# Kernel optimization log

Hardware: AMD Instinct MI355X
Metric: run time of the kernel (lower is better)

Reference implementation:

```python
import jax, jax.numpy as jnp
import numpy as np

N = 100000        # nodes
E = 1_600_000     # edges (avg degree 16)
F_IN = 128        # in_channels
HID = 64          # hidden_channels (per-head)
H1 = 4            # heads layer 1
G = 128           # number of graphs
NEG_SLOPE = 0.2   # PyG GATConv default leaky_relu slope


def setup_inputs() -> dict:
    key = jax.random.key(0)
    ks = jax.random.split(key, 12)
    x = jax.random.normal(ks[0], (N, F_IN), dtype=jnp.float32)
    edge_index = jax.random.randint(ks[1], (2, E), 0, N, dtype=jnp.int64)
    batch = jnp.sort(jax.random.randint(ks[2], (N,), 0, G, dtype=jnp.int64))
    s1 = 1.0 / np.sqrt(F_IN)
    s2 = 1.0 / np.sqrt(H1 * HID)
    # layer 1: in=F_IN, out=H1*HID (PyG lin has no bias; separate bias after concat)
    w1 = jax.random.normal(ks[3], (H1 * HID, F_IN), dtype=jnp.float32) * s1
    a_src1 = jax.random.normal(ks[4], (H1, HID), dtype=jnp.float32) * s1
    a_dst1 = jax.random.normal(ks[5], (H1, HID), dtype=jnp.float32) * s1
    b1 = jnp.zeros((H1 * HID,), dtype=jnp.float32)
    # layer 2: in=H1*HID, out=HID, heads=1
    w2 = jax.random.normal(ks[6], (1 * HID, H1 * HID), dtype=jnp.float32) * s2
    a_src2 = jax.random.normal(ks[7], (1, HID), dtype=jnp.float32) * s2
    a_dst2 = jax.random.normal(ks[8], (1, HID), dtype=jnp.float32) * s2
    b2 = jnp.zeros((HID,), dtype=jnp.float32)
    return {"x": x, "w1": w1, "a_src1": a_src1, "a_dst1": a_dst1, "b1": b1,
            "w2": w2, "a_src2": a_src2, "a_dst2": a_dst2, "b2": b2,
            "edge_index": edge_index, "batch": batch}


def _segment_softmax(alpha, seg, n):
    # numerically-stable softmax of alpha [E,H] grouped by seg (dst node)
    m = jax.ops.segment_max(alpha, seg, num_segments=n)
    m = jnp.where(jnp.isfinite(m), m, 0.0)  # empty segments -> 0
    a = jnp.exp(alpha - m[seg])
    s = jax.ops.segment_sum(a, seg, num_segments=n)
    return a / (s[seg] + 1e-16)


def _gat_conv(x, w, a_src, a_dst, bias, src, dst, n, heads, ch):
    h = (x @ w.T).reshape(n, heads, ch)          # [N,H,C]
    alpha_src = jnp.sum(h * a_src[None], axis=-1)  # [N,H]
    alpha_dst = jnp.sum(h * a_dst[None], axis=-1)  # [N,H]
    e = jax.nn.leaky_relu(alpha_src[src] + alpha_dst[dst], NEG_SLOPE)  # [E,H]
    att = _segment_softmax(e, dst, n)             # [E,H]
    msg = h[src] * att[:, :, None]                # [E,H,C]
    out = jax.ops.segment_sum(msg, dst, num_segments=n)  # [N,H,C]
    return out.reshape(n, heads * ch) + bias


def reference(x, w1, a_src1, a_dst1, b1, w2, a_src2, a_dst2, b2, edge_index, batch):
    src, dst = edge_index[0], edge_index[1]
    h = jax.nn.relu(_gat_conv(x, w1, a_src1, a_dst1, b1, src, dst, N, H1, HID))
    h = jax.nn.relu(_gat_conv(h, w2, a_src2, a_dst2, b2, src, dst, N, 1, HID))
    # global_mean_pool over graph ids
    sums = jax.ops.segment_sum(h, batch, num_segments=G)            # [G,HID]
    cnt = jax.ops.segment_sum(jnp.ones((N,), h.dtype), batch, num_segments=G)
    return sums / jnp.maximum(cnt, 1.0)[:, None]
```

## Files before the change

### kernel.cpp

```cpp
#include <hip/hip_runtime.h>
#include <math.h>
#include <type_traits>

#define NNODES 100000
#define NEDGES 1600000
#define NGRAPH 128
#define NBKT 391
#define CAP 1536
#define EPB 2048

typedef _Float16 f16x4 __attribute__((ext_vector_type(4)));
typedef _Float16 f16x8 __attribute__((ext_vector_type(8)));
typedef float f32x4 __attribute__((ext_vector_type(4)));

__global__ void convert_w(const float* __restrict__ w1, const float* __restrict__ w2,
                          _Float16* __restrict__ w1h, _Float16* __restrict__ w2h) {
  int i = blockIdx.x * 256 + threadIdx.x;
  if (i < 256 * 128) w1h[i] = (_Float16)w1[i];
  int j = i - 256 * 128;
  if (j >= 0 && j < 64 * 256) w2h[j] = (_Float16)w2[j];
}

template <int K, int N, int BN, typename AT>
__global__ __launch_bounds__(256) void gemm_mfma(const AT* __restrict__ A,
    const _Float16* __restrict__ Bh, _Float16* __restrict__ C, int M,
    const float* __restrict__ a_src, const float* __restrict__ a_dst,
    float* __restrict__ asrc, float* __restrict__ adst) {
  constexpr int H = N / 64;
  constexpr int HB = BN / 64;
  constexpr int KS = K / 32, NT = BN / 16;
  const int lane = threadIdx.x & 63, wid = threadIdx.x >> 6;
  const int lr = lane & 15;
  const int lk = (lane >> 4) * 8;
  const int row = blockIdx.x * 64 + wid * 16 + lr;
  const int bn0 = blockIdx.y * BN;
  const int hoff = blockIdx.y * HB;

  f16x8 a[KS];
  if (row < M) {
    const AT* arow = A + (size_t)row * K;
#pragma unroll
    for (int ks = 0; ks < KS; ++ks) {
      if constexpr (std::is_same<AT, float>::value) {
        float4 v0 = *(const float4*)&arow[ks * 32 + lk];
        float4 v1 = *(const float4*)&arow[ks * 32 + lk + 4];
        f16x8 t;
        t[0] = (_Float16)v0.x; t[1] = (_Float16)v0.y; t[2] = (_Float16)v0.z; t[3] = (_Float16)v0.w;
        t[4] = (_Float16)v1.x; t[5] = (_Float16)v1.y; t[6] = (_Float16)v1.z; t[7] = (_Float16)v1.w;
        a[ks] = t;
      } else {
        a[ks] = *(const f16x8*)&arow[ks * 32 + lk];
      }
    }
  } else {
#pragma unroll
    for (int ks = 0; ks < KS; ++ks) a[ks] = (f16x8){};
  }

  f32x4 acc[NT];
#pragma unroll
  for (int nt = 0; nt < NT; ++nt) acc[nt] = (f32x4){0.f, 0.f, 0.f, 0.f};

#pragma unroll
  for (int nt = 0; nt < NT; ++nt) {
    const _Float16* brow = Bh + (size_t)(bn0 + nt * 16 + lr) * K;
#pragma unroll
    for (int ks = 0; ks < KS; ++ks) {
      f16x8 b = *(const f16x8*)&brow[ks * 32 + lk];
      acc[nt] = __builtin_amdgcn_mfma_f32_16x16x32_f16(a[ks], b, acc[nt], 0, 0, 0);
    }
  }

  float cs[NT], cd[NT];
#pragma unroll
  for (int nt = 0; nt < NT; ++nt) {
    cs[nt] = a_src[bn0 + nt * 16 + lr];
    cd[nt] = a_dst[bn0 + nt * 16 + lr];
  }

  int row0 = blockIdx.x * 64 + wid * 16 + (lane >> 4) * 4;
#pragma unroll
  for (int r = 0; r < 4; ++r) {
    int orow = row0 + r;
    float ps[HB], pd[HB];
#pragma unroll
    for (int h = 0; h < HB; ++h) { ps[h] = 0.f; pd[h] = 0.f; }
#pragma unroll
    for (int nt = 0; nt < NT; ++nt) {
      int h = (HB == 1) ? 0 : (nt >> 2);
      ps[h] = fmaf(acc[nt][r], cs[nt], ps[h]);
      pd[h] = fmaf(acc[nt][r], cd[nt], pd[h]);
    }
#pragma unroll
    for (int o = 1; o < 16; o <<= 1) {
#pragma unroll
      for (int h = 0; h < HB; ++h) {
        ps[h] += __shfl_xor(ps[h], o);
        pd[h] += __shfl_xor(pd[h], o);
      }
    }
    if (orow < M) {
#pragma unroll
      for (int nt = 0; nt < NT; ++nt)
        C[(size_t)orow * N + bn0 + nt * 16 + lr] = (_Float16)acc[nt][r];
      if (lr == 0) {
#pragma unroll
        for (int h = 0; h < HB; ++h) {
          asrc[orow * H + hoff + h] = ps[h];
          adst[orow * H + hoff + h] = pd[h];
        }
      }
    }
  }
}

__global__ __launch_bounds__(256) void bucketA(const int* __restrict__ srcv,
    const int* __restrict__ dstv, int2* __restrict__ part, int* __restrict__ gcur,
    int e_count) {
  __shared__ int hist[NBKT];
  __shared__ int base_[NBKT];
  __shared__ int lofs[NBKT];
  const int tid = threadIdx.x;
  const int P = blockIdx.x & 7;
  for (int i = tid; i < NBKT; i += 256) { hist[i] = 0; lofs[i] = 0; }
  __syncthreads();
  const int e0 = blockIdx.x * EPB;
  const int e1 = min(e0 + EPB, e_count);
  for (int e = e0 + tid; e < e1; e += 256) atomicAdd(&hist[dstv[e] >> 8], 1);
  __syncthreads();
  for (int i = tid; i < NBKT; i += 256) {
    int c = hist[i];
    base_[i] = c ? atomicAdd(&gcur[(P * NBKT + i) * 16], c) : 0;
  }
  __syncthreads();
  for (int e = e0 + tid; e < e1; e += 256) {
    int d = dstv[e];
    int b = d >> 8;
    int l = atomicAdd(&lofs[b], 1);
    part[(size_t)(P * NBKT + b) * CAP + base_[b] + l] = make_int2(srcv[e], d);
  }
}

__global__ __launch_bounds__(256) void bucketB1(const int2* __restrict__ part,
    const int* __restrict__ gcur, int* __restrict__ deg, int n) {
  __shared__ int cnt[256];
  const int b = blockIdx.x;
  const int tid = threadIdx.x;
  cnt[tid] = 0;
  __syncthreads();
  for (int P = 0; P < 8; ++P) {
    int cn = gcur[(P * NBKT + b) * 16];
    const int2* seg = part + (size_t)(P * NBKT + b) * CAP;
    for (int i = tid; i < cn; i += 256) atomicAdd(&cnt[seg[i].y & 255], 1);
  }
  __syncthreads();
  int node = (b << 8) + tid;
  if (node < n) deg[node] = cnt[tid];
}

__global__ __launch_bounds__(256) void bucketB2(const int2* __restrict__ part,
    const int* __restrict__ gcur, const int* __restrict__ offsets,
    int* __restrict__ esrc, int n) {
  __shared__ int lcur[256];
  const int b = blockIdx.x;
  const int tid = threadIdx.x;
  int node = (b << 8) + tid;
  lcur[tid] = (node < n) ? offsets[node] : 0;
  __syncthreads();
  for (int P = 0; P < 8; ++P) {
    int cn = gcur[(P * NBKT + b) * 16];
    const int2* seg = part + (size_t)(P * NBKT + b) * CAP;
    for (int i = tid; i < cn; i += 256) {
      int2 e = seg[i];
      int slot = atomicAdd(&lcur[e.y & 255], 1);
      esrc[slot] = e.x;
    }
  }
}

__global__ __launch_bounds__(1024) void scan1(const int* __restrict__ deg, int* __restrict__ inc,
                                              int* __restrict__ bsum, int n) {
  __shared__ int sm[1024];
  int i = blockIdx.x * 1024 + threadIdx.x;
  sm[threadIdx.x] = (i < n) ? deg[i] : 0;
  __syncthreads();
  for (int o = 1; o < 1024; o <<= 1) {
    int t = (threadIdx.x >= o) ? sm[threadIdx.x - o] : 0;
    __syncthreads();
    sm[threadIdx.x] += t;
    __syncthreads();
  }
  if (i < n) inc[i] = sm[threadIdx.x];
  if (threadIdx.x == 1023) bsum[blockIdx.x] = sm[1023];
}

__global__ void scan2(const int* __restrict__ bsum, int* __restrict__ boff, int nb) {
  __shared__ int sm[128];
  int t = threadIdx.x;
  int own = (t < nb) ? bsum[t] : 0;
  sm[t] = own;
  __syncthreads();
  for (int o = 1; o < 128; o <<= 1) {
    int u = (t >= o) ? sm[t - o] : 0;
    __syncthreads();
    sm[t] += u;
    __syncthreads();
  }
  if (t < nb) boff[t] = sm[t] - own;
}

__global__ void scan3(const int* __restrict__ inc, const int* __restrict__ deg,
                      const int* __restrict__ boff, int* __restrict__ offsets,
                      int n, int e_count) {
  int i = blockIdx.x * blockDim.x + threadIdx.x;
  if (i < n) offsets[i] = inc[i] - deg[i] + boff[i >> 10];
  if (i == 0) offsets[n] = e_count;
}

__global__ __launch_bounds__(256) void agg1_kernel(const _Float16* __restrict__ hmat,
    const float* __restrict__ asrc, const float* __restrict__ adst,
    const int* __restrict__ offsets, const int* __restrict__ esrc,
    const float* __restrict__ bias, _Float16* __restrict__ outv, int node0, int node_end) {
  const int lane = threadIdx.x & 63, wid = threadIdx.x >> 6;
  const int node = node0 + blockIdx.x * 4 + wid;
  if (node >= node_end) return;
  const int h = lane >> 4;
  const int start = offsets[node];
  const int end = offsets[node + 1];
  const float adn = adst[node * 4 + h];
  const _Float16* hbase = hmat + lane * 4;
  float acc[4] = {0.f, 0.f, 0.f, 0.f};
  float s = 0.f;
  int j = start;
  for (; j + 8 <= end; j += 8) {
    int sv[8];
#pragma unroll
    for (int t = 0; t < 8; ++t) sv[t] = esrc[j + t];
    f16x4 vv[8];
#pragma unroll
    for (int t = 0; t < 8; ++t) vv[t] = *(const f16x4*)&hbase[(size_t)sv[t] * 256];
    _Float16 ph[8];
#pragma unroll
    for (int t = 0; t < 8; ++t) {
      float v = asrc[sv[t] * 4 + h] + adn;
      v = (v > 0.f) ? v : 0.2f * v;
      float p = __expf(v);
      s += p;
      ph[t] = (_Float16)p;
    }
#pragma unroll
    for (int t = 0; t < 8; ++t)
#pragma unroll
      for (int k = 0; k < 4; ++k)
        acc[k] = fmaf((float)vv[t][k], (float)ph[t], acc[k]);
  }
  for (; j < end; ++j) {
    int sv = esrc[j];
    f16x4 vv = *(const f16x4*)&hbase[(size_t)sv * 256];
    float v = asrc[sv * 4 + h] + adn;
    v = (v > 0.f) ? v : 0.2f * v;
    float p = __expf(v);
    s += p;
    _Float16 phs = (_Float16)p;
#pragma unroll
    for (int k = 0; k < 4; ++k) acc[k] = fmaf((float)vv[k], (float)phs, acc[k]);
  }
  float inv = 1.f / (s + 1e-16f);
  f16x4 ho;
#pragma unroll
  for (int k = 0; k < 4; ++k)
    ho[k] = (_Float16)fmaxf(fmaf(acc[k], inv, bias[lane * 4 + k]), 0.f);
  *(f16x4*)&outv[(size_t)node * 256 + lane * 4] = ho;
}

__global__ __launch_bounds__(256) void agg2_kernel(const _Float16* __restrict__ hmat,
    const float* __restrict__ asrc, const float* __restrict__ adst,
    const int* __restrict__ offsets, const int* __restrict__ esrc,
    const float* __restrict__ bias, float* __restrict__ outv) {
  const int lane = threadIdx.x & 63, wid = threadIdx.x >> 6;
  const int g = lane >> 4, q = lane & 15;
  const int node = blockIdx.x * 16 + wid * 4 + g;
  if (node >= NNODES) return;
  const int start = offsets[node];
  const int end = offsets[node + 1];
  const float adn = adst[node];
  const _Float16* hbase = hmat + q * 4;
  float acc[4] = {0.f, 0.f, 0.f, 0.f};
  float s = 0.f;
  int j = start;
  for (; j + 4 <= end; j += 4) {
    int sv[4];
#pragma unroll
    for (int t = 0; t < 4; ++t) sv[t] = esrc[j + t];
    f16x4 v[4];
#pragma unroll
    for (int t = 0; t < 4; ++t) v[t] = *(const f16x4*)&hbase[(size_t)sv[t] * 64];
#pragma unroll
    for (int t = 0; t < 4; ++t) {
      float x = asrc[sv[t]] + adn;
      x = (x > 0.f) ? x : 0.2f * x;
      float p = __expf(x);
      s += p;
      _Float16 phs = (_Float16)p;
#pragma unroll
      for (int k = 0; k < 4; ++k) acc[k] = fmaf((float)v[t][k], (float)phs, acc[k]);
    }
  }
  for (; j < end; ++j) {
    int sv = esrc[j];
    f16x4 v = *(const f16x4*)&hbase[(size_t)sv * 64];
    float x = asrc[sv] + adn;
    x = (x > 0.f) ? x : 0.2f * x;
    float p = __expf(x);
    s += p;
    _Float16 phs = (_Float16)p;
#pragma unroll
    for (int k = 0; k < 4; ++k) acc[k] = fmaf((float)v[k], (float)phs, acc[k]);
  }
  float inv = 1.f / (s + 1e-16f);
  float4 o;
  o.x = fmaxf(fmaf(acc[0], inv, bias[q * 4 + 0]), 0.f);
  o.y = fmaxf(fmaf(acc[1], inv, bias[q * 4 + 1]), 0.f);
  o.z = fmaxf(fmaf(acc[2], inv, bias[q * 4 + 2]), 0.f);
  o.w = fmaxf(fmaf(acc[3], inv, bias[q * 4 + 3]), 0.f);
  *(float4*)&outv[(size_t)node * 64 + q * 4] = o;
}

__global__ __launch_bounds__(256) void pool_kernel(const float* __restrict__ g2,
    const int* __restrict__ batch, float* __restrict__ out, int n) {
  const int gid = blockIdx.x;
  const int lane = threadIdx.x & 63, w = threadIdx.x >> 6;
  int lo = 0, hi = n;
  while (lo < hi) { int mid = (lo + hi) >> 1; if (batch[mid] < gid) lo = mid + 1; else hi = mid; }
  int lb = lo;
  hi = n;
  while (lo < hi) { int mid = (lo + hi) >> 1; if (batch[mid] < gid + 1) lo = mid + 1; else hi = mid; }
  int ub = lo;
  float acc = 0.f;
  for (int i = lb + w; i < ub; i += 4) acc += g2[(size_t)i * 64 + lane];
  __shared__ float red[4][64];
  red[w][lane] = acc;
  __syncthreads();
  if (threadIdx.x < 64) {
    float sum = (red[0][lane] + red[1][lane]) + (red[2][lane] + red[3][lane]);
    float cnt = fmaxf((float)(ub - lb), 1.f);
    out[gid * 64 + lane] = sum / cnt;
  }
}

extern "C" void kernel_launch(void* const* d_in, const int* in_sizes, int n_in,
                              void* d_out, int out_size, void* d_ws, size_t ws_size,
                              hipStream_t stream) {
  const float* x      = (const float*)d_in[0];
  const float* w1     = (const float*)d_in[1];
  const float* a_src1 = (const float*)d_in[2];
  const float* a_dst1 = (const float*)d_in[3];
  const float* b1     = (const float*)d_in[4];
  const float* w2     = (const float*)d_in[5];
  const float* a_src2 = (const float*)d_in[6];
  const float* a_dst2 = (const float*)d_in[7];
  const float* b2     = (const float*)d_in[8];
  const int*   src    = (const int*)d_in[9];
  const int*   dst    = src + NEDGES;
  const int*   batch  = (const int*)d_in[10];
  float* out = (float*)d_out;

  const int N = NNODES, E = NEDGES;
  const int NB = (N + 1023) / 1024;

  char* wsb = (char*)d_ws;
  size_t off = 0;
  auto alloc = [&](size_t bytes) {
    void* p = wsb + off;
    off = (off + bytes + 255) & ~(size_t)255;
    return p;
  };
  _Float16* h1h = (_Float16*)alloc((size_t)N * 256 * 2);
  _Float16* g1h = (_Float16*)alloc((size_t)N * 256 * 2);
  _Float16* h2h = (_Float16*)alloc((size_t)N * 64 * 2);
  float* g2     = (float*)alloc((size_t)N * 64 * 4);
  float* as1    = (float*)alloc((size_t)N * 4 * 4);
  float* ad1    = (float*)alloc((size_t)N * 4 * 4);
  float* as2    = (float*)alloc((size_t)N * 4);
  float* ad2    = (float*)alloc((size_t)N * 4);
  int* deg      = (int*)alloc((size_t)N * 4);
  int* inc      = (int*)alloc((size_t)N * 4);
  int* bsum     = (int*)alloc((size_t)NB * 4);
  int* boff     = (int*)alloc((size_t)NB * 4);
  int* offsets  = (int*)alloc((size_t)(N + 1) * 4);
  int* esrc     = (int*)alloc((size_t)E * 4);
  int2* part    = (int2*)alloc((size_t)8 * NBKT * CAP * 8);
  int* gcur     = (int*)alloc((size_t)8 * NBKT * 16 * 4);
  _Float16* w1h = (_Float16*)alloc((size_t)256 * 128 * 2);
  _Float16* w2h = (_Float16*)alloc((size_t)64 * 256 * 2);

  convert_w<<<192, 256, 0, stream>>>(w1, w2, w1h, w2h);

  hipMemsetAsync(gcur, 0, (size_t)8 * NBKT * 16 * 4, stream);
  bucketA<<<(E + EPB - 1) / EPB, 256, 0, stream>>>(src, dst, part, gcur, E);
  bucketB1<<<NBKT, 256, 0, stream>>>(part, gcur, deg, N);
  scan1<<<NB, 1024, 0, stream>>>(deg, inc, bsum, N);
  scan2<<<1, 128, 0, stream>>>(bsum, boff, NB);
  scan3<<<(N + 255) / 256, 256, 0, stream>>>(inc, deg, boff, offsets, N, E);
  bucketB2<<<NBKT, 256, 0, stream>>>(part, gcur, offsets, esrc, N);

  {
    dim3 g((N + 63) / 64, 2);
    gemm_mfma<128, 256, 128, float><<<g, 256, 0, stream>>>(
        x, w1h, h1h, N, a_src1, a_dst1, as1, ad1);
  }
  agg1_kernel<<<8334, 256, 0, stream>>>(h1h, as1, ad1, offsets, esrc, b1, g1h, 0, 33336);
  agg1_kernel<<<8334, 256, 0, stream>>>(h1h, as1, ad1, offsets, esrc, b1, g1h, 33336, 66672);
  agg1_kernel<<<8332, 256, 0, stream>>>(h1h, as1, ad1, offsets, esrc, b1, g1h, 66672, 100000);

  {
    dim3 g((N + 63) / 64, 1);
    gemm_mfma<256, 64, 64, _Float16><<<g, 256, 0, stream>>>(
        g1h, w2h, h2h, N, a_src2, a_dst2, as2, ad2);
  }
  agg2_kernel<<<(N + 15) / 16, 256, 0, stream>>>(h2h, as2, ad2, offsets, esrc, b2, g2);

  pool_kernel<<<NGRAPH, 256, 0, stream>>>(g2, batch, out, N);
}
```

Measured before the change: 414.2 us.

## Fold attention vectors into weight matrix and compute scores with an extra MFMA tile

Precomputes W^T·a_src and W^T·a_dst as extra fp16 columns so the per-node attention logits come from one additional MFMA tile instead of a shuffle-reduced epilogue. The layer-1 GEMM is no longer split across two column blocks, so each block loads the x row once and computes all 256 outputs. The three chunked agg1 launches are merged into one. The logits now come from fp16 folded vectors, which changes rounding slightly, and each thread holds more accumulators.

```diff
diff --git a/kernel.cpp b/kernel.cpp
--- a/kernel.cpp
+++ b/kernel.cpp
@@ -14,27 +14,43 @@
 typedef float f32x4 __attribute__((ext_vector_type(4)));
 
 __global__ void convert_w(const float* __restrict__ w1, const float* __restrict__ w2,
-                          _Float16* __restrict__ w1h, _Float16* __restrict__ w2h) {
-  int i = blockIdx.x * 256 + threadIdx.x;
-  if (i < 256 * 128) w1h[i] = (_Float16)w1[i];
-  int j = i - 256 * 128;
-  if (j >= 0 && j < 64 * 256) w2h[j] = (_Float16)w2[j];
-}
-
-template <int K, int N, int BN, typename AT>
+                          const float* __restrict__ as1c, const float* __restrict__ ad1c,
+                          const float* __restrict__ as2c, const float* __restrict__ ad2c,
+                          _Float16* __restrict__ w1h, _Float16* __restrict__ w2h,
+                          _Float16* __restrict__ va1, _Float16* __restrict__ va2) {
+  const int b = blockIdx.x, tid = threadIdx.x;
+  if (b < 8) {
+    if (tid >= 128) return;
+    int h = b & 3;
+    const float* coef = (b >= 4) ? ad1c : as1c;
+    float s = 0.f;
+    for (int c = 0; c < 64; ++c) s = fmaf(w1[(size_t)(h * 64 + c) * 128 + tid], coef[h * 64 + c], s);
+    va1[b * 128 + tid] = (_Float16)s;
+  } else if (b < 10) {
+    int r = b - 8;
+    const float* coef = r ? ad2c : as2c;
+    float s = 0.f;
+    for (int c = 0; c < 64; ++c) s = fmaf(w2[(size_t)c * 256 + tid], coef[c], s);
+    va2[r * 256 + tid] = (_Float16)s;
+  } else if (b < 138) {
+    int i = (b - 10) * 256 + tid;
+    w1h[i] = (_Float16)w1[i];
+  } else {
+    int i = (b - 138) * 256 + tid;
+    w2h[i] = (_Float16)w2[i];
+  }
+}
+
+template <int K, int N, typename AT>
 __global__ __launch_bounds__(256) void gemm_mfma(const AT* __restrict__ A,
-    const _Float16* __restrict__ Bh, _Float16* __restrict__ C, int M,
-    const float* __restrict__ a_src, const float* __restrict__ a_dst,
-    float* __restrict__ asrc, float* __restrict__ adst) {
+    const _Float16* __restrict__ Bh, const _Float16* __restrict__ VA,
+    _Float16* __restrict__ C, int M, float* __restrict__ asrc, float* __restrict__ adst) {
   constexpr int H = N / 64;
-  constexpr int HB = BN / 64;
-  constexpr int KS = K / 32, NT = BN / 16;
+  constexpr int KS = K / 32, NT = N / 16;
   const int lane = threadIdx.x & 63, wid = threadIdx.x >> 6;
   const int lr = lane & 15;
   const int lk = (lane >> 4) * 8;
   const int row = blockIdx.x * 64 + wid * 16 + lr;
-  const int bn0 = blockIdx.y * BN;
-  const int hoff = blockIdx.y * HB;
 
   f16x8 a[KS];
   if (row < M) {
@@ -57,13 +73,22 @@
     for (int ks = 0; ks < KS; ++ks) a[ks] = (f16x8){};
   }
 
+  f32x4 accv = (f32x4){0.f, 0.f, 0.f, 0.f};
+  {
+    const _Float16* vrow = VA + (size_t)lr * K;
+#pragma unroll
+    for (int ks = 0; ks < KS; ++ks) {
+      f16x8 b = *(const f16x8*)&vrow[ks * 32 + lk];
+      accv = __builtin_amdgcn_mfma_f32_16x16x32_f16(a[ks], b, accv, 0, 0, 0);
+    }
+  }
+
   f32x4 acc[NT];
 #pragma unroll
   for (int nt = 0; nt < NT; ++nt) acc[nt] = (f32x4){0.f, 0.f, 0.f, 0.f};
-
 #pragma unroll
   for (int nt = 0; nt < NT; ++nt) {
-    const _Float16* brow = Bh + (size_t)(bn0 + nt * 16 + lr) * K;
+    const _Float16* brow = Bh + (size_t)(nt * 16 + lr) * K;
 #pragma unroll
     for (int ks = 0; ks < KS; ++ks) {
       f16x8 b = *(const f16x8*)&brow[ks * 32 + lk];
@@ -71,46 +96,16 @@
     }
   }
 
-  float cs[NT], cd[NT];
-#pragma unroll
-  for (int nt = 0; nt < NT; ++nt) {
-    cs[nt] = a_src[bn0 + nt * 16 + lr];
-    cd[nt] = a_dst[bn0 + nt * 16 + lr];
-  }
-
   int row0 = blockIdx.x * 64 + wid * 16 + (lane >> 4) * 4;
 #pragma unroll
   for (int r = 0; r < 4; ++r) {
     int orow = row0 + r;
-    float ps[HB], pd[HB];
-#pragma unroll
-    for (int h = 0; h < HB; ++h) { ps[h] = 0.f; pd[h] = 0.f; }
-#pragma unroll
-    for (int nt = 0; nt < NT; ++nt) {
-      int h = (HB == 1) ? 0 : (nt >> 2);
-      ps[h] = fmaf(acc[nt][r], cs[nt], ps[h]);
-      pd[h] = fmaf(acc[nt][r], cd[nt], pd[h]);
-    }
-#pragma unroll
-    for (int o = 1; o < 16; o <<= 1) {
-#pragma unroll
-      for (int h = 0; h < HB; ++h) {
-        ps[h] += __shfl_xor(ps[h], o);
-        pd[h] += __shfl_xor(pd[h], o);
-      }
-    }
-    if (orow < M) {
-#pragma unroll
-      for (int nt = 0; nt < NT; ++nt)
-        C[(size_t)orow * N + bn0 + nt * 16 + lr] = (_Float16)acc[nt][r];
-      if (lr == 0) {
-#pragma unroll
-        for (int h = 0; h < HB; ++h) {
-          asrc[orow * H + hoff + h] = ps[h];
-          adst[orow * H + hoff + h] = pd[h];
-        }
-      }
-    }
+    if (orow >= M) continue;
+#pragma unroll
+    for (int nt = 0; nt < NT; ++nt)
+      C[(size_t)orow * N + nt * 16 + lr] = (_Float16)acc[nt][r];
+    if (lr < H) asrc[orow * H + lr] = accv[r];
+    else if (lr < 2 * H) adst[orow * H + lr - H] = accv[r];
   }
 }
 
@@ -220,10 +215,10 @@
 __global__ __launch_bounds__(256) void agg1_kernel(const _Float16* __restrict__ hmat,
     const float* __restrict__ asrc, const float* __restrict__ adst,
     const int* __restrict__ offsets, const int* __restrict__ esrc,
-    const float* __restrict__ bias, _Float16* __restrict__ outv, int node0, int node_end) {
+    const float* __restrict__ bias, _Float16* __restrict__ outv) {
   const int lane = threadIdx.x & 63, wid = threadIdx.x >> 6;
-  const int node = node0 + blockIdx.x * 4 + wid;
-  if (node >= node_end) return;
+  const int node = blockIdx.x * 4 + wid;
+  if (node >= NNODES) return;
   const int h = lane >> 4;
   const int start = offsets[node];
   const int end = offsets[node + 1];
@@ -393,8 +388,13 @@
   int* gcur     = (int*)alloc((size_t)8 * NBKT * 16 * 4);
   _Float16* w1h = (_Float16*)alloc((size_t)256 * 128 * 2);
   _Float16* w2h = (_Float16*)alloc((size_t)64 * 256 * 2);
-
-  convert_w<<<192, 256, 0, stream>>>(w1, w2, w1h, w2h);
+  _Float16* va1 = (_Float16*)alloc((size_t)16 * 128 * 2);
+  _Float16* va2 = (_Float16*)alloc((size_t)16 * 256 * 2);
+
+  hipMemsetAsync(va1, 0, (size_t)16 * 128 * 2, stream);
+  hipMemsetAsync(va2, 0, (size_t)16 * 256 * 2, stream);
+  convert_w<<<202, 256, 0, stream>>>(w1, w2, a_src1, a_dst1, a_src2, a_dst2,
+                                     w1h, w2h, va1, va2);
 
   hipMemsetAsync(gcur, 0, (size_t)8 * NBKT * 16 * 4, stream);
   bucketA<<<(E + EPB - 1) / EPB, 256, 0, stream>>>(src, dst, part, gcur, E);
@@ -404,20 +404,12 @@
   scan3<<<(N + 255) / 256, 256, 0, stream>>>(inc, deg, boff, offsets, N, E);
   bucketB2<<<NBKT, 256, 0, stream>>>(part, gcur, offsets, esrc, N);
 
-  {
-    dim3 g((N + 63) / 64, 2);
-    gemm_mfma<128, 256, 128, float><<<g, 256, 0, stream>>>(
-        x, w1h, h1h, N, a_src1, a_dst1, as1, ad1);
-  }
-  agg1_kernel<<<8334, 256, 0, stream>>>(h1h, as1, ad1, offsets, esrc, b1, g1h, 0, 33336);
-  agg1_kernel<<<8334, 256, 0, stream>>>(h1h, as1, ad1, offsets, esrc, b1, g1h, 33336, 66672);
-  agg1_kernel<<<8332, 256, 0, stream>>>(h1h, as1, ad1, offsets, esrc, b1, g1h, 66672, 100000);
-
-  {
-    dim3 g((N + 63) / 64, 1);
-    gemm_mfma<256, 64, 64, _Float16><<<g, 256, 0, stream>>>(
-        g1h, w2h, h2h, N, a_src2, a_dst2, as2, ad2);
-  }
+  gemm_mfma<128, 256, float><<<(N + 63) / 64, 256, 0, stream>>>(
+      x, w1h, va1, h1h, N, as1, ad1);
+  agg1_kernel<<<(N + 3) / 4, 256, 0, stream>>>(h1h, as1, ad1, offsets, esrc, b1, g1h);
+
+  gemm_mfma<256, 64, _Float16><<<(N + 63) / 64, 256, 0, stream>>>(
+      g1h, w2h, va2, h2h, N, as2, ad2);
   agg2_kernel<<<(N + 15) / 16, 256, 0, stream>>>(h2h, as2, ad2, offsets, esrc, b2, g2);
 
   pool_kernel<<<NGRAPH, 256, 0, stream>>>(g2, batch, out, N);
```

Result: no change. 411.2 us (-0.7%).
